# Kernel optimization log

Hardware: AMD Instinct MI355X
Metric: run time of the kernel (lower is better)

## Reference

```python
import jax, jax.numpy as jnp
import numpy as np

B, S, V, E, H, L = 16, 1024, 32000, 512, 512, 10  # batch, seq, vocab, emb, lstm hidden, labels


def setup_inputs() -> dict:
    key = jax.random.key(0)
    ks = jax.random.split(key, 24)
    s = 1.0 / np.sqrt(H)
    u = lambda k, shape: jax.random.uniform(k, shape, jnp.float32, -s, s)
    inp = {}
    inp['emb'] = jax.random.normal(ks[0], (V, E), jnp.float32) * 0.1
    # layer 0 (input E), layer 1 (input 2H), each with fwd + reverse direction
    names = [('l0', E), ('l0r', E), ('l1', 2 * H), ('l1r', 2 * H)]
    for j, (nm, din) in enumerate(names):
        base = 1 + 4 * j
        inp['w_ih_' + nm] = u(ks[base + 0], (4 * H, din))
        inp['w_hh_' + nm] = u(ks[base + 1], (4 * H, H))
        inp['b_ih_' + nm] = u(ks[base + 2], (4 * H,))
        inp['b_hh_' + nm] = u(ks[base + 3], (4 * H,))
    inp['out_w'] = u(ks[20], (L, 2 * H))
    inp['out_b'] = u(ks[21], (L,))
    inp['tokens'] = jax.random.randint(ks[22], (B, S), 0, V)
    return inp


def lstm_layer(x, w_ih, w_hh, b_ih, b_hh, reverse):
    # x: (B, S, Din) -> (B, S, H); PyTorch gate order i, f, g, o
    n = x.shape[0]
    h0 = jnp.zeros((n, w_hh.shape[1]), x.dtype)

    def step(carry, xt):
        h, c = carry
        g = xt @ w_ih.T + h @ w_hh.T + b_ih + b_hh
        i, f, gg, o = jnp.split(g, 4, axis=-1)
        i, f, o = jax.nn.sigmoid(i), jax.nn.sigmoid(f), jax.nn.sigmoid(o)
        c = f * c + i * jnp.tanh(gg)
        h = o * jnp.tanh(c)
        return (h, c), h

    _, hs = jax.lax.scan(step, (h0, h0), jnp.swapaxes(x, 0, 1), reverse=reverse)
    return jnp.swapaxes(hs, 0, 1)


def masked_softmax(scores, mask):
    # softmax over last axis restricted to columns where mask[b, t] is True;
    # zero probabilities if the group is empty (matches torch empty-matmul -> 0)
    neg = jnp.where(mask[:, None, :], scores, -jnp.inf)
    m = jnp.max(neg, axis=-1, keepdims=True)
    m = jnp.where(jnp.isfinite(m), m, 0.0)
    e = jnp.exp(neg - m)
    d = jnp.sum(e, axis=-1, keepdims=True)
    return jnp.where(d > 0, e / jnp.where(d > 0, d, 1.0), 0.0)


def reference(tokens, emb, w_ih_l0, w_hh_l0, b_ih_l0, b_hh_l0,
              w_ih_l0r, w_hh_l0r, b_ih_l0r, b_hh_l0r,
              w_ih_l1, w_hh_l1, b_ih_l1, b_hh_l1,
              w_ih_l1r, w_hh_l1r, b_ih_l1r, b_hh_l1r,
              out_w, out_b):
    x = emb[tokens]  # (B, S, E)
    x = jnp.concatenate([
        lstm_layer(x, w_ih_l0, w_hh_l0, b_ih_l0, b_hh_l0, False),
        lstm_layer(x, w_ih_l0r, w_hh_l0r, b_ih_l0r, b_hh_l0r, True)], axis=-1)
    x = jnp.concatenate([
        lstm_layer(x, w_ih_l1, w_hh_l1, b_ih_l1, b_hh_l1, False),
        lstm_layer(x, w_ih_l1r, w_hh_l1r, b_ih_l1r, b_hh_l1r, True)], axis=-1)  # (B,S,2H)
    result = x @ out_w.T + out_b  # (B, S, L)
    tags = jnp.argmax(result, axis=2)
    me = tags != 0  # 'entity' group; complement is the 'other' group
    scores = jnp.einsum('bsd,btd->bst', x, x)  # (B, S, S)
    P = masked_softmax(scores, me) + masked_softmax(scores, ~me)
    A = jnp.einsum('bst,btd->bsd', P, x) + x  # Ae@He + Ao@Ho + H
    return (A, result)
```

## Files before the change

### kernel.cpp

```cpp
#include <hip/hip_runtime.h>

#define B_ 16
#define S_ 1024
#define H_ 512
#define E_ 512
#define L_ 10

typedef float f4_t __attribute__((ext_vector_type(4)));
typedef __attribute__((address_space(1))) void gas_void;
typedef __attribute__((address_space(3))) void las_void;

__device__ __forceinline__ float frcp_(float x)
{
    float r;
    asm("v_rcp_f32 %0, %1" : "=v"(r) : "v"(x));
    return r;
}
__device__ __forceinline__ float fsig_(float x) { return frcp_(1.0f + __expf(-x)); }
__device__ __forceinline__ float ftanh_(float x)
{
    const float e = __expf(-2.0f * fabsf(x));
    const float r = (1.0f - e) * frcp_(1.0f + e);
    return copysignf(r, x);
}

__device__ __forceinline__ void store_wt4(float* p, f4_t v)
{
    asm volatile("global_store_dwordx4 %0, %1, off sc0 sc1" :: "v"(p), "v"(v) : "memory");
}

__device__ __forceinline__ void gll16(const float* g, float* l)
{
    __builtin_amdgcn_global_load_lds((const gas_void*)g, (las_void*)l, 16, 0, 0);
}

__global__ __launch_bounds__(128) void embed_kernel(const int* __restrict__ tokens,
                                                    const float* __restrict__ emb,
                                                    float* __restrict__ x0)
{
    const int row = blockIdx.x;
    const int tok = tokens[row];
    const float4* src = (const float4*)(emb + (size_t)tok * E_);
    float4* dst = (float4*)(x0 + (size_t)row * E_);
    dst[threadIdx.x] = src[threadIdx.x];
}

#define GLL_TILE(DST, SRC, RS)                                      \
    _Pragma("unroll")                                               \
    for (int k = 0; k < 8; ++k) {                                   \
        const int m_  = (wvi << 3) | k;                             \
        const int rr_ = m_ >> 1;                                    \
        const int ch_ = (m_ & 1) << 8;                              \
        gll16((SRC) + (size_t)rr_ * (RS) + ch_ + lane * 4,          \
              (DST) + rr_ * 516 + ch_);                             \
    }

#define EG8(PP, WEXPR)                                                        \
    _Pragma("unroll")                                                         \
    for (int cc = 0; cc < 8; ++cc) {                                          \
        const int scol = kb + (((cc + ks) & 7) << 2);                         \
        const float4 hv0 = *(const float4*)&(PP)[(b40 + 0) * 516 + scol];     \
        const float4 hv1 = *(const float4*)&(PP)[(b40 + 1) * 516 + scol];     \
        const float4 hv2 = *(const float4*)&(PP)[(b40 + 2) * 516 + scol];     \
        const float4 hv3 = *(const float4*)&(PP)[(b40 + 3) * 516 + scol];     \
        _Pragma("unroll")                                                     \
        for (int j = 0; j < 4; ++j) {                                         \
            const float4 wv = (WEXPR);                                        \
            acc[j*4+0] = fmaf(wv.x, hv0.x, acc[j*4+0]);                       \
            acc[j*4+0] = fmaf(wv.y, hv0.y, acc[j*4+0]);                       \
            acc[j*4+0] = fmaf(wv.z, hv0.z, acc[j*4+0]);                       \
            acc[j*4+0] = fmaf(wv.w, hv0.w, acc[j*4+0]);                       \
            acc[j*4+1] = fmaf(wv.x, hv1.x, acc[j*4+1]);                       \
            acc[j*4+1] = fmaf(wv.y, hv1.y, acc[j*4+1]);                       \
            acc[j*4+1] = fmaf(wv.z, hv1.z, acc[j*4+1]);                       \
            acc[j*4+1] = fmaf(wv.w, hv1.w, acc[j*4+1]);                       \
            acc[j*4+2] = fmaf(wv.x, hv2.x, acc[j*4+2]);                       \
            acc[j*4+2] = fmaf(wv.y, hv2.y, acc[j*4+2]);                       \
            acc[j*4+2] = fmaf(wv.z, hv2.z, acc[j*4+2]);                       \
            acc[j*4+2] = fmaf(wv.w, hv2.w, acc[j*4+2]);                       \
            acc[j*4+3] = fmaf(wv.x, hv3.x, acc[j*4+3]);                       \
            acc[j*4+3] = fmaf(wv.y, hv3.y, acc[j*4+3]);                       \
            acc[j*4+3] = fmaf(wv.z, hv3.z, acc[j*4+3]);                       \
            acc[j*4+3] = fmaf(wv.w, hv3.w, acc[j*4+3]);                       \
        }                                                                     \
    }

template<int DIN>
__global__ __launch_bounds__(256, 1) void lstm_bidir(
    const float* __restrict__ x,
    const float* __restrict__ wihF, const float* __restrict__ whhF,
    const float* __restrict__ bihF, const float* __restrict__ bhhF,
    const float* __restrict__ wihR, const float* __restrict__ whhR,
    const float* __restrict__ bihR, const float* __restrict__ bhhR,
    float* __restrict__ hs,
    int* __restrict__ flags)
{
    constexpr int NH = DIN / 512;

    const int tid = threadIdx.x;
    const int bid = blockIdx.x;
    const int dir = bid >> 7;
    const int c0  = (bid & 127) << 2;

    const float* wih = dir ? wihR : wihF;
    const float* whh = dir ? whhR : whhF;
    const float* bih = dir ? bihR : bihF;
    const float* bhh = dir ? bhhR : bhhF;

    __shared__ __align__(16) float s_wih[16 * 516];
    __shared__ __align__(16) float s_whh[16 * 516];
    __shared__ __align__(16) float s_P[16 * 516];
    __shared__ __align__(16) float s_Q[16 * 516];
    __shared__ __align__(16) float s_red[4][16][20];
    __shared__ float s_bias[16];

    for (int r = 0; r < 16; ++r) {
        const int grow = ((r >> 2) * H_) + c0 + (r & 3);
        const float* srcI = wih + (size_t)grow * DIN;
        for (int i = tid; i < 128; i += 256)
            *(float4*)&s_wih[r * 516 + i * 4] = *(const float4*)&srcI[i * 4];
        const float* srcH = whh + (size_t)grow * H_;
        for (int i = tid; i < 128; i += 256)
            *(float4*)&s_whh[r * 516 + i * 4] = *(const float4*)&srcH[i * 4];
    }
    if (tid < 16) {
        const int grow = ((tid >> 2) * H_) + c0 + (tid & 3);
        s_bias[tid] = bih[grow] + bhh[grow];
    }

    const int rb   = tid & 15;
    const int ks   = tid >> 4;
    const int r40  = (rb >> 2) << 2;
    const int b40  = (rb & 3) << 2;
    const int kb   = ks << 5;
    const int lane = tid & 63;
    const int wvi  = tid >> 6;
    const int pfl  = (dir * 128 + (tid & 127)) << 4;

    float cstate = 0.0f;
    float acc[16];

    {
        const int t0 = dir ? (S_ - 1) : 0;
        GLL_TILE(s_P, x + (size_t)t0 * DIN, (size_t)S_ * DIN);
        if (NH == 2) GLL_TILE(s_Q, x + (size_t)t0 * DIN + 512, (size_t)S_ * DIN);
    }

    for (int step = 0; step < S_; ++step) {
        const int t  = dir ? (S_ - 1 - step) : step;
        const int sn = (step + 1 < S_) ? (step + 1) : (S_ - 1);
        const int tn = dir ? (S_ - 1 - sn) : sn;
        const int tp = dir ? (t + 1) : (t - 1);

        asm volatile("s_waitcnt vmcnt(0)" ::: "memory");
        __syncthreads();

        if (step > 0) {
            if (tid == 0)
                __hip_atomic_store(&flags[bid << 4], step,
                                   __ATOMIC_RELAXED, __HIP_MEMORY_SCOPE_AGENT);
            int* fp = &flags[pfl];
            while (__hip_atomic_load(fp, __ATOMIC_RELAXED, __HIP_MEMORY_SCOPE_AGENT) < step) { }
            asm volatile("" ::: "memory");
        }

        #pragma unroll
        for (int a = 0; a < 16; ++a) acc[a] = 0.0f;

        if constexpr (NH == 2) {
            EG8(s_Q, (*(const float4*)&wih[(size_t)((r40 >> 2) * H_ + c0 + j) * DIN + 512 + scol]));
            __syncthreads();
            if (step > 0)
                GLL_TILE(s_Q, hs + (size_t)tp * 1024 + dir * 512, (size_t)S_ * 1024);
            EG8(s_P, (*(const float4*)&s_wih[(r40 + j) * 516 + scol]));
            asm volatile("s_waitcnt vmcnt(0)" ::: "memory");
            __syncthreads();
            GLL_TILE(s_P, x + (size_t)tn * DIN, (size_t)S_ * DIN);
            if (step > 0)
                EG8(s_Q, (*(const float4*)&s_whh[(r40 + j) * 516 + scol]));
        } else {
            if (step > 0)
                GLL_TILE(s_Q, hs + (size_t)tp * 1024 + dir * 512, (size_t)S_ * 1024);
            EG8(s_P, (*(const float4*)&s_wih[(r40 + j) * 516 + scol]));
            asm volatile("s_waitcnt vmcnt(0)" ::: "memory");
            __syncthreads();
            GLL_TILE(s_P, x + (size_t)tn * DIN, (size_t)S_ * DIN);
            if (step > 0)
                EG8(s_Q, (*(const float4*)&s_whh[(r40 + j) * 516 + scol]));
        }

        #pragma unroll
        for (int a = 0; a < 16; ++a) {
            float v = acc[a];
            v += __shfl_xor(v, 16);
            v += __shfl_xor(v, 32);
            acc[a] = v;
        }
        if ((tid & 63) < 16) {
            float* base = &s_red[wvi][tid & 15][0];
            #pragma unroll
            for (int q = 0; q < 4; ++q)
                *(float4*)&base[q * 4] =
                    make_float4(acc[q * 4 + 0], acc[q * 4 + 1], acc[q * 4 + 2], acc[q * 4 + 3]);
        }
        __syncthreads();

        if (tid < 64) {
            const int c = tid >> 4, b = tid & 15;
            float g[4];
            #pragma unroll
            for (int gg = 0; gg < 4; ++gg) {
                const int rbv = (gg << 2) | (b >> 2);
                const int av  = (c << 2) | (b & 3);
                g[gg] = s_bias[gg * 4 + c]
                      + s_red[0][rbv][av] + s_red[1][rbv][av]
                      + s_red[2][rbv][av] + s_red[3][rbv][av];
            }
            const float iv = fsig_(g[0]);
            const float fv = fsig_(g[1]);
            const float gv = ftanh_(g[2]);
            const float ov = fsig_(g[3]);
            cstate = fv * cstate + iv * gv;
            const float hval = ov * ftanh_(cstate);
            f4_t o;
            o.x = hval;
            o.y = __shfl(hval, tid + 16);
            o.z = __shfl(hval, tid + 32);
            o.w = __shfl(hval, tid + 48);
            if (tid < 16)
                store_wt4(&hs[(size_t)(b * S_ + t) * 1024 + dir * 512 + c0], o);
        }
        if (NH == 2)
            GLL_TILE(s_Q, x + (size_t)tn * DIN + 512, (size_t)S_ * DIN);
    }
}

__global__ __launch_bounds__(256) void outproj_kernel(
    const float* __restrict__ x1, const float* __restrict__ out_w,
    const float* __restrict__ out_b, float* __restrict__ res,
    unsigned char* __restrict__ mask)
{
    const int tid  = threadIdx.x;
    const int lane = tid & 63;
    const int w    = tid >> 6;
    const int row  = blockIdx.x * 4 + w;
    const float* xr = x1 + (size_t)row * 1024;
    float4 xv[4];
    #pragma unroll
    for (int i = 0; i < 4; ++i) xv[i] = *(const float4*)&xr[(i * 64 + lane) << 2];
    float best = -__builtin_inff();
    int bi = 0;
    #pragma unroll
    for (int l = 0; l < L_; ++l) {
        const float* wr = out_w + l * 1024;
        float s = 0.0f;
        #pragma unroll
        for (int i = 0; i < 4; ++i) {
            const float4 wv = *(const float4*)&wr[(i * 64 + lane) << 2];
            s = fmaf(xv[i].x, wv.x, s);
            s = fmaf(xv[i].y, wv.y, s);
            s = fmaf(xv[i].z, wv.z, s);
            s = fmaf(xv[i].w, wv.w, s);
        }
        #pragma unroll
        for (int d = 32; d >= 1; d >>= 1) s += __shfl_xor(s, d);
        s += out_b[l];
        if (lane == l) res[(size_t)row * L_ + l] = s;
        if (s > best) { best = s; bi = l; }
    }
    if (lane == 0) mask[row] = (unsigned char)(bi != 0);
}

template<int MODE>
__global__ __launch_bounds__(256) void gemm64(
    const float* __restrict__ A, const float* __restrict__ Bm,
    const float* __restrict__ D, float* __restrict__ C,
    const int M, const int N, const int K)
{
    const int bz = blockIdx.z;
    const float* Ab = A  + (size_t)bz * M * K;
    const float* Bb = Bm + (size_t)bz * N * K;
    const float* Db = (MODE == 1) ? (D + (size_t)bz * M * N) : (const float*)nullptr;
    float* Cb = C + (size_t)bz * M * N;
    const int m0 = blockIdx.y << 6;
    const int n0 = blockIdx.x << 6;
    const int tid = threadIdx.x;
    const int tm = tid >> 4, tn = tid & 15;
    const int am = tid >> 2, ak = (tid & 3) << 2;
    const int bk1 = tid >> 4, bn1 = (tid & 15) << 2;
    __shared__ float As[16][68];
    __shared__ float Bs[16][68];
    float acc[4][4] = {};
    for (int k0 = 0; k0 < K; k0 += 16) {
        const float4 av = *(const float4*)&Ab[(size_t)(m0 + am) * K + k0 + ak];
        float4 bv;
        if (MODE == 0) bv = *(const float4*)&Bb[(size_t)(n0 + am) * K + k0 + ak];
        else           bv = *(const float4*)&Bb[(size_t)(k0 + bk1) * N + n0 + bn1];
        __syncthreads();
        As[ak + 0][am] = av.x; As[ak + 1][am] = av.y;
        As[ak + 2][am] = av.z; As[ak + 3][am] = av.w;
        if (MODE == 0) {
            Bs[ak + 0][am] = bv.x; Bs[ak + 1][am] = bv.y;
            Bs[ak + 2][am] = bv.z; Bs[ak + 3][am] = bv.w;
        } else {
            *(float4*)&Bs[bk1][bn1] = bv;
        }
        __syncthreads();
        #pragma unroll
        for (int k = 0; k < 16; ++k) {
            const float4 a4 = *(const float4*)&As[k][tm << 2];
            const float4 b4 = *(const float4*)&Bs[k][tn << 2];
            acc[0][0] = fmaf(a4.x, b4.x, acc[0][0]); acc[0][1] = fmaf(a4.x, b4.y, acc[0][1]);
            acc[0][2] = fmaf(a4.x, b4.z, acc[0][2]); acc[0][3] = fmaf(a4.x, b4.w, acc[0][3]);
            acc[1][0] = fmaf(a4.y, b4.x, acc[1][0]); acc[1][1] = fmaf(a4.y, b4.y, acc[1][1]);
            acc[1][2] = fmaf(a4.y, b4.z, acc[1][2]); acc[1][3] = fmaf(a4.y, b4.w, acc[1][3]);
            acc[2][0] = fmaf(a4.z, b4.x, acc[2][0]); acc[2][1] = fmaf(a4.z, b4.y, acc[2][1]);
            acc[2][2] = fmaf(a4.z, b4.z, acc[2][2]); acc[2][3] = fmaf(a4.z, b4.w, acc[2][3]);
            acc[3][0] = fmaf(a4.w, b4.x, acc[3][0]); acc[3][1] = fmaf(a4.w, b4.y, acc[3][1]);
            acc[3][2] = fmaf(a4.w, b4.z, acc[3][2]); acc[3][3] = fmaf(a4.w, b4.w, acc[3][3]);
        }
    }
    #pragma unroll
    for (int j = 0; j < 4; ++j) {
        const size_t ci = (size_t)(m0 + (tm << 2) + j) * N + n0 + (tn << 2);
        float4 o = make_float4(acc[j][0], acc[j][1], acc[j][2], acc[j][3]);
        if (MODE == 1) {
            const float4 dv = *(const float4*)&Db[ci];
            o.x += dv.x; o.y += dv.y; o.z += dv.z; o.w += dv.w;
        }
        *(float4*)&Cb[ci] = o;
    }
}

__global__ __launch_bounds__(256) void softmax_kernel(float* __restrict__ sc,
                                                      const unsigned char* __restrict__ mask)
{
    const float INF = __builtin_inff();
    const int row = blockIdx.x;
    const int b = row >> 10;
    float* pr = sc + (size_t)row * 1024;
    const unsigned char* mr = mask + b * 1024;
    const int tid = threadIdx.x;
    const int lane = tid & 63;
    const int w = tid >> 6;
    const int j0 = tid << 2;
    const float4 v = *(const float4*)&pr[j0];
    const unsigned mu = *(const unsigned*)&mr[j0];
    const bool m0 = (mu & 0xffu) != 0, m1 = ((mu >> 8) & 0xffu) != 0;
    const bool m2 = ((mu >> 16) & 0xffu) != 0, m3 = ((mu >> 24) & 0xffu) != 0;

    float mme = -INF, mot = -INF;
    if (m0) mme = fmaxf(mme, v.x); else mot = fmaxf(mot, v.x);
    if (m1) mme = fmaxf(mme, v.y); else mot = fmaxf(mot, v.y);
    if (m2) mme = fmaxf(mme, v.z); else mot = fmaxf(mot, v.z);
    if (m3) mme = fmaxf(mme, v.w); else mot = fmaxf(mot, v.w);
    #pragma unroll
    for (int d = 32; d >= 1; d >>= 1) {
        mme = fmaxf(mme, __shfl_xor(mme, d));
        mot = fmaxf(mot, __shfl_xor(mot, d));
    }
    __shared__ float sm[2][4];
    if (lane == 0) { sm[0][w] = mme; sm[1][w] = mot; }
    __syncthreads();
    float Mme = fmaxf(fmaxf(sm[0][0], sm[0][1]), fmaxf(sm[0][2], sm[0][3]));
    float Mot = fmaxf(fmaxf(sm[1][0], sm[1][1]), fmaxf(sm[1][2], sm[1][3]));
    const float MmeU = (Mme == -INF) ? 0.0f : Mme;
    const float MotU = (Mot == -INF) ? 0.0f : Mot;

    const float e0 = expf(v.x - (m0 ? MmeU : MotU));
    const float e1 = expf(v.y - (m1 ? MmeU : MotU));
    const float e2 = expf(v.z - (m2 ? MmeU : MotU));
    const float e3 = expf(v.w - (m3 ? MmeU : MotU));
    float sme = 0.0f, sot = 0.0f;
    if (m0) sme += e0; else sot += e0;
    if (m1) sme += e1; else sot += e1;
    if (m2) sme += e2; else sot += e2;
    if (m3) sme += e3; else sot += e3;
    #pragma unroll
    for (int d = 32; d >= 1; d >>= 1) {
        sme += __shfl_xor(sme, d);
        sot += __shfl_xor(sot, d);
    }
    __syncthreads();
    if (lane == 0) { sm[0][w] = sme; sm[1][w] = sot; }
    __syncthreads();
    const float Dme = sm[0][0] + sm[0][1] + sm[0][2] + sm[0][3];
    const float Dot = sm[1][0] + sm[1][1] + sm[1][2] + sm[1][3];

    float4 o;
    o.x = m0 ? (Dme > 0.0f ? e0 / Dme : 0.0f) : (Dot > 0.0f ? e0 / Dot : 0.0f);
    o.y = m1 ? (Dme > 0.0f ? e1 / Dme : 0.0f) : (Dot > 0.0f ? e1 / Dot : 0.0f);
    o.z = m2 ? (Dme > 0.0f ? e2 / Dme : 0.0f) : (Dot > 0.0f ? e2 / Dot : 0.0f);
    o.w = m3 ? (Dme > 0.0f ? e3 / Dme : 0.0f) : (Dot > 0.0f ? e3 / Dot : 0.0f);
    *(float4*)&pr[j0] = o;
}

extern "C" void kernel_launch(void* const* d_in, const int* in_sizes, int n_in,
                              void* d_out, int out_size, void* d_ws, size_t ws_size,
                              hipStream_t stream)
{
    const float* emb     = (const float*)d_in[0];
    const float* wih_l0  = (const float*)d_in[1];
    const float* whh_l0  = (const float*)d_in[2];
    const float* bih_l0  = (const float*)d_in[3];
    const float* bhh_l0  = (const float*)d_in[4];
    const float* wih_l0r = (const float*)d_in[5];
    const float* whh_l0r = (const float*)d_in[6];
    const float* bih_l0r = (const float*)d_in[7];
    const float* bhh_l0r = (const float*)d_in[8];
    const float* wih_l1  = (const float*)d_in[9];
    const float* whh_l1  = (const float*)d_in[10];
    const float* bih_l1  = (const float*)d_in[11];
    const float* bhh_l1  = (const float*)d_in[12];
    const float* wih_l1r = (const float*)d_in[13];
    const float* whh_l1r = (const float*)d_in[14];
    const float* bih_l1r = (const float*)d_in[15];
    const float* bhh_l1r = (const float*)d_in[16];
    const float* out_w   = (const float*)d_in[17];
    const float* out_b   = (const float*)d_in[18];
    const int*   tokens  = (const int*)d_in[19];

    float* out     = (float*)d_out;
    float* A_out   = out;
    float* res_out = out + 16777216;

    float* ws = (float*)d_ws;
    float* x0 = ws;
    float* h0 = ws + 8388608;
    float* x1 = h0 + 16777216;
    float* sc = x1 + 16777216;
    unsigned char* mask = (unsigned char*)(sc + 16777216);
    int* flags0 = (int*)(mask + 16384);
    int* flags1 = flags0 + 256 * 16;

    (void)in_sizes; (void)n_in; (void)out_size; (void)ws_size;

    (void)hipMemsetAsync(flags0, 0, 2 * 256 * 16 * sizeof(int), stream);

    embed_kernel<<<B_ * S_, 128, 0, stream>>>(tokens, emb, x0);

    lstm_bidir<512><<<256, 256, 0, stream>>>(
        x0, wih_l0, whh_l0, bih_l0, bhh_l0,
        wih_l0r, whh_l0r, bih_l0r, bhh_l0r, h0, flags0);

    lstm_bidir<1024><<<256, 256, 0, stream>>>(
        h0, wih_l1, whh_l1, bih_l1, bhh_l1,
        wih_l1r, whh_l1r, bih_l1r, bhh_l1r, x1, flags1);

    outproj_kernel<<<(B_ * S_) / 4, 256, 0, stream>>>(x1, out_w, out_b, res_out, mask);

    dim3 gg(16, 16, 16);
    gemm64<0><<<gg, 256, 0, stream>>>(x1, x1, nullptr, sc, 1024, 1024, 1024);

    softmax_kernel<<<B_ * S_, 256, 0, stream>>>(sc, mask);

    gemm64<1><<<gg, 256, 0, stream>>>(sc, x1, x1, A_out, 1024, 1024, 1024);
}
```

Before: 14.34 ms.

## Replace flag-based inter-block LSTM sync with NaN-sentinel polling on hidden state

Before the LSTM kernels run, the hidden-state buffers are pre-filled with NaN sentinels, and the per-block flag counters are removed. Each block now loads the previous timestep's hidden values directly with cache-bypassing loads and spins until none of them are NaN. This removes the separate flag store and flag poll from every recurrent step, cutting per-step cross-block latency. The costs are an extra fill pass over two large buffers, and a hang if a real hidden value is ever NaN.

Result: slower. 40.40 ms (+181.6%).

```diff
diff --git a/kernel.cpp b/kernel.cpp
--- a/kernel.cpp
+++ b/kernel.cpp
@@ -32,6 +32,19 @@
 __device__ __forceinline__ void gll16(const float* g, float* l)
 {
     __builtin_amdgcn_global_load_lds((const gas_void*)g, (las_void*)l, 16, 0, 0);
+}
+
+#define WAITV0() asm volatile("s_waitcnt vmcnt(0)" ::: "memory")
+#define WAITV8() asm volatile("s_waitcnt vmcnt(8)" ::: "memory")
+#define WAITV9() asm volatile("s_waitcnt vmcnt(9)" ::: "memory")
+#define BAR() do { asm volatile("s_waitcnt lgkmcnt(0)" ::: "memory"); \
+                   __builtin_amdgcn_s_barrier(); } while (0)
+
+__global__ __launch_bounds__(256) void fill_sentinel(unsigned int* p, long n4)
+{
+    const uint4 v = make_uint4(~0u, ~0u, ~0u, ~0u);
+    for (long j = (long)blockIdx.x * 256 + threadIdx.x; j < n4; j += (long)gridDim.x * 256)
+        ((uint4*)p)[j] = v;
 }
 
 __global__ __launch_bounds__(128) void embed_kernel(const int* __restrict__ tokens,
@@ -85,6 +98,16 @@
         }                                                                     \
     }
 
+#define PLOAD(I) asm volatile("global_load_dwordx4 %0, %1, off sc0 sc1"       \
+        : "=v"(hv##I) : "v"(hbase + (size_t)(I) * 2097152) : "memory")
+#define PLOAD_ALL  PLOAD(0); PLOAD(1); PLOAD(2); PLOAD(3);                    \
+                   PLOAD(4); PLOAD(5); PLOAD(6); PLOAD(7)
+#define NAN4(V) (((V).x != (V).x) | ((V).y != (V).y) |                        \
+                 ((V).z != (V).z) | ((V).w != (V).w))
+#define NAN_ALL (NAN4(hv0) | NAN4(hv1) | NAN4(hv2) | NAN4(hv3) |              \
+                 NAN4(hv4) | NAN4(hv5) | NAN4(hv6) | NAN4(hv7))
+#define HSTAGE(I) *(f4_t*)&s_Q[(((I) << 1) + row0) * 516 + cst] = hv##I
+
 template<int DIN>
 __global__ __launch_bounds__(256, 1) void lstm_bidir(
     const float* __restrict__ x,
@@ -92,8 +115,7 @@
     const float* __restrict__ bihF, const float* __restrict__ bhhF,
     const float* __restrict__ wihR, const float* __restrict__ whhR,
     const float* __restrict__ bihR, const float* __restrict__ bhhR,
-    float* __restrict__ hs,
-    int* __restrict__ flags)
+    float* __restrict__ hs)
 {
     constexpr int NH = DIN / 512;
 
@@ -133,9 +155,10 @@
     const int r40  = (rb >> 2) << 2;
     const int b40  = (rb & 3) << 2;
     const int kb   = ks << 5;
+    const int cst  = (tid & 127) << 2;
+    const int row0 = tid >> 7;
     const int lane = tid & 63;
     const int wvi  = tid >> 6;
-    const int pfl  = (dir * 128 + (tid & 127)) << 4;
 
     float cstate = 0.0f;
     float acc[16];
@@ -151,42 +174,46 @@
         const int sn = (step + 1 < S_) ? (step + 1) : (S_ - 1);
         const int tn = dir ? (S_ - 1 - sn) : sn;
         const int tp = dir ? (t + 1) : (t - 1);
-
-        asm volatile("s_waitcnt vmcnt(0)" ::: "memory");
-        __syncthreads();
+        const float* hbase = hs + ((size_t)row0 * S_ + (size_t)(step > 0 ? tp : 0)) * 1024
+                                + dir * 512 + cst;
+
+        f4_t hv0, hv1, hv2, hv3, hv4, hv5, hv6, hv7;
+        if (step > 0) { PLOAD_ALL; }
 
         if (step > 0) {
-            if (tid == 0)
-                __hip_atomic_store(&flags[bid << 4], step,
-                                   __ATOMIC_RELAXED, __HIP_MEMORY_SCOPE_AGENT);
-            int* fp = &flags[pfl];
-            while (__hip_atomic_load(fp, __ATOMIC_RELAXED, __HIP_MEMORY_SCOPE_AGENT) < step) { }
-            asm volatile("" ::: "memory");
-        }
+            if (NH == 1 && wvi == 0) { WAITV9(); } else { WAITV8(); }
+        } else { WAITV0(); }
+        BAR();
 
         #pragma unroll
         for (int a = 0; a < 16; ++a) acc[a] = 0.0f;
 
+        EG8(s_P, (*(const float4*)&s_wih[(r40 + j) * 516 + scol]));
         if constexpr (NH == 2) {
             EG8(s_Q, (*(const float4*)&wih[(size_t)((r40 >> 2) * H_ + c0 + j) * DIN + 512 + scol]));
-            __syncthreads();
-            if (step > 0)
-                GLL_TILE(s_Q, hs + (size_t)tp * 1024 + dir * 512, (size_t)S_ * 1024);
-            EG8(s_P, (*(const float4*)&s_wih[(r40 + j) * 516 + scol]));
-            asm volatile("s_waitcnt vmcnt(0)" ::: "memory");
-            __syncthreads();
-            GLL_TILE(s_P, x + (size_t)tn * DIN, (size_t)S_ * DIN);
-            if (step > 0)
-                EG8(s_Q, (*(const float4*)&s_whh[(r40 + j) * 516 + scol]));
-        } else {
-            if (step > 0)
-                GLL_TILE(s_Q, hs + (size_t)tp * 1024 + dir * 512, (size_t)S_ * 1024);
-            EG8(s_P, (*(const float4*)&s_wih[(r40 + j) * 516 + scol]));
-            asm volatile("s_waitcnt vmcnt(0)" ::: "memory");
-            __syncthreads();
-            GLL_TILE(s_P, x + (size_t)tn * DIN, (size_t)S_ * DIN);
-            if (step > 0)
-                EG8(s_Q, (*(const float4*)&s_whh[(r40 + j) * 516 + scol]));
+        }
+
+        if (step > 0) {
+            WAITV0();
+            __builtin_amdgcn_sched_barrier(0);
+            bool bad = NAN_ALL;
+            while (bad) {
+                asm volatile("s_sleep 2" ::: "memory");
+                PLOAD_ALL;
+                WAITV0();
+                __builtin_amdgcn_sched_barrier(0);
+                bad = NAN_ALL;
+            }
+        }
+        BAR();
+
+        if (step > 0) { HSTAGE(0); HSTAGE(1); HSTAGE(2); HSTAGE(3);
+                        HSTAGE(4); HSTAGE(5); HSTAGE(6); HSTAGE(7); }
+        GLL_TILE(s_P, x + (size_t)tn * DIN, (size_t)S_ * DIN);
+        BAR();
+
+        if (step > 0) {
+            EG8(s_Q, (*(const float4*)&s_whh[(r40 + j) * 516 + scol]));
         }
 
         #pragma unroll
@@ -203,7 +230,7 @@
                 *(float4*)&base[q * 4] =
                     make_float4(acc[q * 4 + 0], acc[q * 4 + 1], acc[q * 4 + 2], acc[q * 4 + 3]);
         }
-        __syncthreads();
+        BAR();
 
         if (tid < 64) {
             const int c = tid >> 4, b = tid & 15;
@@ -230,7 +257,7 @@
             if (tid < 16)
                 store_wt4(&hs[(size_t)(b * S_ + t) * 1024 + dir * 512 + c0], o);
         }
-        if (NH == 2)
+        if constexpr (NH == 2)
             GLL_TILE(s_Q, x + (size_t)tn * DIN + 512, (size_t)S_ * DIN);
     }
 }
@@ -430,22 +457,20 @@
     float* x1 = h0 + 16777216;
     float* sc = x1 + 16777216;
     unsigned char* mask = (unsigned char*)(sc + 16777216);
-    int* flags0 = (int*)(mask + 16384);
-    int* flags1 = flags0 + 256 * 16;
 
     (void)in_sizes; (void)n_in; (void)out_size; (void)ws_size;
 
-    (void)hipMemsetAsync(flags0, 0, 2 * 256 * 16 * sizeof(int), stream);
+    fill_sentinel<<<2048, 256, 0, stream>>>((unsigned int*)h0, 8388608L);
 
     embed_kernel<<<B_ * S_, 128, 0, stream>>>(tokens, emb, x0);
 
     lstm_bidir<512><<<256, 256, 0, stream>>>(
         x0, wih_l0, whh_l0, bih_l0, bhh_l0,
-        wih_l0r, whh_l0r, bih_l0r, bhh_l0r, h0, flags0);
+        wih_l0r, whh_l0r, bih_l0r, bhh_l0r, h0);
 
     lstm_bidir<1024><<<256, 256, 0, stream>>>(
         h0, wih_l1, whh_l1, bih_l1, bhh_l1,
-        wih_l1r, whh_l1r, bih_l1r, bhh_l1r, x1, flags1);
+        wih_l1r, whh_l1r, bih_l1r, bhh_l1r, x1);
 
     outproj_kernel<<<(B_ * S_) / 4, 256, 0, stream>>>(x1, out_w, out_b, res_out, mask);
 
```

## Move grid flag polling after input-projection work and pack flags densely

Applied to the files above, without the earlier changes.

The per-step cross-block flag wait in the persistent bidirectional LSTM kernel now happens after part of the input-weight GEMV work, so other blocks' progress overlaps with local computation. Flags are packed contiguously, one int per block instead of one per 64-byte slot, and each thread polls two of them instead of one padded slot. __syncthreads is replaced by an explicit lgkmcnt wait plus s_barrier. Packing the flags means many blocks' flags share cache lines, which may add contention between stores and polls. Deferring the wait also changes the ordering between the flag store and the hs reads, which needs care for correctness.

After: 14.70 ms. 1.02x slower.

```diff
diff --git a/kernel.cpp b/kernel.cpp
--- a/kernel.cpp
+++ b/kernel.cpp
@@ -33,6 +33,10 @@
 {
     __builtin_amdgcn_global_load_lds((const gas_void*)g, (las_void*)l, 16, 0, 0);
 }
+
+#define WAITV0() asm volatile("s_waitcnt vmcnt(0)" ::: "memory")
+#define BAR() do { asm volatile("s_waitcnt lgkmcnt(0)" ::: "memory"); \
+                   __builtin_amdgcn_s_barrier(); } while (0)
 
 __global__ __launch_bounds__(128) void embed_kernel(const int* __restrict__ tokens,
                                                     const float* __restrict__ emb,
@@ -55,9 +59,9 @@
               (DST) + rr_ * 516 + ch_);                             \
     }
 
-#define EG8(PP, WEXPR)                                                        \
+#define EG4(PP, WEXPR, CB)                                                    \
     _Pragma("unroll")                                                         \
-    for (int cc = 0; cc < 8; ++cc) {                                          \
+    for (int cc = (CB); cc < (CB) + 4; ++cc) {                                \
         const int scol = kb + (((cc + ks) & 7) << 2);                         \
         const float4 hv0 = *(const float4*)&(PP)[(b40 + 0) * 516 + scol];     \
         const float4 hv1 = *(const float4*)&(PP)[(b40 + 1) * 516 + scol];     \
@@ -84,6 +88,18 @@
             acc[j*4+3] = fmaf(wv.w, hv3.w, acc[j*4+3]);                       \
         }                                                                     \
     }
+#define EG8(PP, WEXPR) EG4(PP, WEXPR, 0) EG4(PP, WEXPR, 4)
+
+#define POLL2()                                                               \
+    do {                                                                      \
+        int* fp0_ = &flags[(dir << 7) + (tid & 63)];                          \
+        int* fp1_ = fp0_ + 64;                                                \
+        while (__hip_atomic_load(fp0_, __ATOMIC_RELAXED,                      \
+                                 __HIP_MEMORY_SCOPE_AGENT) < step ||          \
+               __hip_atomic_load(fp1_, __ATOMIC_RELAXED,                      \
+                                 __HIP_MEMORY_SCOPE_AGENT) < step) { }        \
+        asm volatile("" ::: "memory");                                        \
+    } while (0)
 
 template<int DIN>
 __global__ __launch_bounds__(256, 1) void lstm_bidir(
@@ -135,7 +151,6 @@
     const int kb   = ks << 5;
     const int lane = tid & 63;
     const int wvi  = tid >> 6;
-    const int pfl  = (dir * 128 + (tid & 127)) << 4;
 
     float cstate = 0.0f;
     float acc[16];
@@ -152,41 +167,39 @@
         const int tn = dir ? (S_ - 1 - sn) : sn;
         const int tp = dir ? (t + 1) : (t - 1);
 
-        asm volatile("s_waitcnt vmcnt(0)" ::: "memory");
-        __syncthreads();
-
-        if (step > 0) {
-            if (tid == 0)
-                __hip_atomic_store(&flags[bid << 4], step,
-                                   __ATOMIC_RELAXED, __HIP_MEMORY_SCOPE_AGENT);
-            int* fp = &flags[pfl];
-            while (__hip_atomic_load(fp, __ATOMIC_RELAXED, __HIP_MEMORY_SCOPE_AGENT) < step) { }
-            asm volatile("" ::: "memory");
-        }
+        WAITV0();
+        BAR();
+        if (step > 0 && tid == 0)
+            __hip_atomic_store(&flags[bid], step,
+                               __ATOMIC_RELAXED, __HIP_MEMORY_SCOPE_AGENT);
 
         #pragma unroll
         for (int a = 0; a < 16; ++a) acc[a] = 0.0f;
 
         if constexpr (NH == 2) {
             EG8(s_Q, (*(const float4*)&wih[(size_t)((r40 >> 2) * H_ + c0 + j) * DIN + 512 + scol]));
-            __syncthreads();
-            if (step > 0)
+            BAR();
+            if (step > 0) {
+                POLL2();
                 GLL_TILE(s_Q, hs + (size_t)tp * 1024 + dir * 512, (size_t)S_ * 1024);
+            }
             EG8(s_P, (*(const float4*)&s_wih[(r40 + j) * 516 + scol]));
-            asm volatile("s_waitcnt vmcnt(0)" ::: "memory");
-            __syncthreads();
-            GLL_TILE(s_P, x + (size_t)tn * DIN, (size_t)S_ * DIN);
-            if (step > 0)
-                EG8(s_Q, (*(const float4*)&s_whh[(r40 + j) * 516 + scol]));
         } else {
-            if (step > 0)
+            EG4(s_P, (*(const float4*)&s_wih[(r40 + j) * 516 + scol]), 0);
+            if (step > 0) {
+                POLL2();
                 GLL_TILE(s_Q, hs + (size_t)tp * 1024 + dir * 512, (size_t)S_ * 1024);
-            EG8(s_P, (*(const float4*)&s_wih[(r40 + j) * 516 + scol]));
-            asm volatile("s_waitcnt vmcnt(0)" ::: "memory");
-            __syncthreads();
-            GLL_TILE(s_P, x + (size_t)tn * DIN, (size_t)S_ * DIN);
-            if (step > 0)
-                EG8(s_Q, (*(const float4*)&s_whh[(r40 + j) * 516 + scol]));
+            }
+            EG4(s_P, (*(const float4*)&s_wih[(r40 + j) * 516 + scol]), 4);
+        }
+
+        WAITV0();
+        BAR();
+
+        GLL_TILE(s_P, x + (size_t)tn * DIN, (size_t)S_ * DIN);
+
+        if (step > 0) {
+            EG8(s_Q, (*(const float4*)&s_whh[(r40 + j) * 516 + scol]));
         }
 
         #pragma unroll
@@ -203,7 +216,7 @@
                 *(float4*)&base[q * 4] =
                     make_float4(acc[q * 4 + 0], acc[q * 4 + 1], acc[q * 4 + 2], acc[q * 4 + 3]);
         }
-        __syncthreads();
+        BAR();
 
         if (tid < 64) {
             const int c = tid >> 4, b = tid & 15;
@@ -230,7 +243,7 @@
             if (tid < 16)
                 store_wt4(&hs[(size_t)(b * S_ + t) * 1024 + dir * 512 + c0], o);
         }
-        if (NH == 2)
+        if constexpr (NH == 2)
             GLL_TILE(s_Q, x + (size_t)tn * DIN + 512, (size_t)S_ * DIN);
     }
 }
@@ -431,11 +444,11 @@
     float* sc = x1 + 16777216;
     unsigned char* mask = (unsigned char*)(sc + 16777216);
     int* flags0 = (int*)(mask + 16384);
-    int* flags1 = flags0 + 256 * 16;
+    int* flags1 = flags0 + 256;
 
     (void)in_sizes; (void)n_in; (void)out_size; (void)ws_size;
 
-    (void)hipMemsetAsync(flags0, 0, 2 * 256 * 16 * sizeof(int), stream);
+    (void)hipMemsetAsync(flags0, 0, 512 * sizeof(int), stream);
 
     embed_kernel<<<B_ * S_, 128, 0, stream>>>(tokens, emb, x0);
 
```
